# Performance work log

Hardware: AMD Instinct MI355X
Metric: run time of the kernel (lower is better)

Reference implementation:

```python
import jax, jax.numpy as jnp
import numpy as np

B, Q, L = 262144, 32, 8


def _rx(theta, ar, ai, br, bi):
    # RX(t) = [[cos(t/2), -i sin(t/2)], [-i sin(t/2), cos(t/2)]]
    c, s = jnp.cos(theta * 0.5), jnp.sin(theta * 0.5)
    return (c * ar + s * bi, c * ai - s * br,
            s * ai + c * br, -s * ar + c * bi)


def _ry(theta, ar, ai, br, bi):
    # RY(t) = [[cos(t/2), -sin(t/2)], [sin(t/2), cos(t/2)]] (real)
    c, s = jnp.cos(theta * 0.5), jnp.sin(theta * 0.5)
    return (c * ar - s * br, c * ai - s * bi,
            s * ar + c * br, s * ai + c * bi)


def _rz(theta, ar, ai, br, bi):
    # RZ(t) = diag(e^{-it/2}, e^{it/2})
    c, s = jnp.cos(theta * 0.5), jnp.sin(theta * 0.5)
    return (c * ar + s * ai, c * ai - s * ar,
            c * br - s * bi, c * bi + s * br)


def setup_inputs() -> dict:
    key = jax.random.key(0)
    k1, k2 = jax.random.split(key)
    x = jax.random.normal(k1, (B, Q), dtype=jnp.float32)
    params = jax.random.normal(k2, (L, Q, 3), dtype=jnp.float32)
    return {"x": x, "params": params}


def reference(x, params):
    # The circuit has only single-qubit gates, so the state factorizes into
    # an independent 2-amplitude state per (batch, qubit); track re/im parts.
    ar = jnp.ones_like(x)          # amplitude of |0>, real part
    ai = jnp.zeros_like(x)
    br = jnp.zeros_like(x)         # amplitude of |1>
    bi = jnp.zeros_like(x)
    # input encoding: RX(x_i) on wire i
    ar, ai, br, bi = _rx(x, ar, ai, br, bi)
    # trainable layers: RY, RZ, RX per qubit (broadcast over batch)
    for layer in range(params.shape[0]):
        ar, ai, br, bi = _ry(params[layer, :, 0][None, :], ar, ai, br, bi)
        ar, ai, br, bi = _rz(params[layer, :, 1][None, :], ar, ai, br, bi)
        ar, ai, br, bi = _rx(params[layer, :, 2][None, :], ar, ai, br, bi)
    # <Z> = |a|^2 - |b|^2 per (batch, qubit)
    return ar * ar + ai * ai - br * br - bi * bi
```

## Files before the change

### kernel.cpp

```cpp
#include <hip/hip_runtime.h>
#include <math.h>

#define NQ 32
#define MAXL 16

typedef float v4f __attribute__((ext_vector_type(4)));

struct Amp { float ar, ai, br, bi; };

__device__ __forceinline__ void g_ry(float c, float s, Amp& v) {
    Amp o;
    o.ar = c * v.ar - s * v.br;
    o.ai = c * v.ai - s * v.bi;
    o.br = s * v.ar + c * v.br;
    o.bi = s * v.ai + c * v.bi;
    v = o;
}
__device__ __forceinline__ void g_rz(float c, float s, Amp& v) {
    Amp o;
    o.ar = c * v.ar + s * v.ai;
    o.ai = c * v.ai - s * v.ar;
    o.br = c * v.br - s * v.bi;
    o.bi = c * v.bi + s * v.br;
    v = o;
}
__device__ __forceinline__ void g_rx(float c, float s, Amp& v) {
    Amp o;
    o.ar = c * v.ar + s * v.bi;
    o.ai = c * v.ai - s * v.br;
    o.br = s * v.ai + c * v.br;
    o.bi = -s * v.ar + c * v.bi;
    v = o;
}

__global__ __launch_bounds__(256, 8) void qc_fused(const float* __restrict__ x,
                                                   const float* __restrict__ params,
                                                   float* __restrict__ out,
                                                   int n4, int L) {
    __shared__ float sTh[MAXL * NQ * 3];
    __shared__ float sK[3][NQ];
    const int t = threadIdx.x;
    const int stride = gridDim.x * blockDim.x;
    const v4f* __restrict__ x4 = reinterpret_cast<const v4f*>(x);
    v4f* __restrict__ out4 = reinterpret_cast<v4f*>(out);

    const int i0 = blockIdx.x * blockDim.x + t;
    const int i1 = i0 + stride, i2 = i1 + stride, i3 = i2 + stride;
    const bool h0 = i0 < n4, h1 = i1 < n4, h2 = i2 < n4, h3 = i3 < n4;
    v4f xa = {0,0,0,0}, xb = {0,0,0,0}, xc = {0,0,0,0}, xd = {0,0,0,0};
    if (h0) xa = x4[i0];
    if (h1) xb = x4[i1];
    if (h2) xc = x4[i2];
    if (h3) xd = x4[i3];

    const int nTh4 = (L * NQ * 3) / 4;
    for (int j = t; j < nTh4; j += blockDim.x)
        reinterpret_cast<v4f*>(sTh)[j] = reinterpret_cast<const v4f*>(params)[j];
    __syncthreads();

    if (t < NQ) {
        Amp e0 = {1.f, 0.f, 0.f, 0.f};
        Amp e1 = {0.f, 0.f, 1.f, 0.f};
        for (int l = 0; l < L; ++l) {
            const float* th = &sTh[(l * NQ + t) * 3];
            float c, s;
            __sincosf(th[0] * 0.5f, &s, &c);
            g_ry(c, s, e0); g_ry(c, s, e1);
            __sincosf(th[1] * 0.5f, &s, &c);
            g_rz(c, s, e0); g_rz(c, s, e1);
            __sincosf(th[2] * 0.5f, &s, &c);
            g_rx(c, s, e0); g_rx(c, s, e1);
        }
        float A = (e0.ar * e0.ar + e0.ai * e0.ai) - (e0.br * e0.br + e0.bi * e0.bi);
        float B = (e1.ar * e1.ar + e1.ai * e1.ai) - (e1.br * e1.br + e1.bi * e1.bi);
        float C = 2.f * ((e0.ar * e1.ai - e0.ai * e1.ar) -
                         (e0.br * e1.bi - e0.bi * e1.br));
        sK[0][t] = 0.5f * (A + B);
        sK[1][t] = 0.5f * (A - B);
        sK[2][t] = 0.5f * C;
    }
    __syncthreads();

    const int q = (4 * t) & (NQ - 1);
    const float k0a = sK[0][q + 0], k1a = sK[1][q + 0], k2a = sK[2][q + 0];
    const float k0b = sK[0][q + 1], k1b = sK[1][q + 1], k2b = sK[2][q + 1];
    const float k0c = sK[0][q + 2], k1c = sK[1][q + 2], k2c = sK[2][q + 2];
    const float k0d = sK[0][q + 3], k1d = sK[1][q + 3], k2d = sK[2][q + 3];

#define EVAL(xv, ov)                                                        \
    do {                                                                    \
        float s_, c_;                                                       \
        __sincosf((xv)[0], &s_, &c_); (ov)[0] = fmaf(k1a, c_, fmaf(k2a, s_, k0a)); \
        __sincosf((xv)[1], &s_, &c_); (ov)[1] = fmaf(k1b, c_, fmaf(k2b, s_, k0b)); \
        __sincosf((xv)[2], &s_, &c_); (ov)[2] = fmaf(k1c, c_, fmaf(k2c, s_, k0c)); \
        __sincosf((xv)[3], &s_, &c_); (ov)[3] = fmaf(k1d, c_, fmaf(k2d, s_, k0d)); \
    } while (0)

    v4f o;
    if (h0) { EVAL(xa, o); __builtin_nontemporal_store(o, out4 + i0); }
    if (h1) { EVAL(xb, o); __builtin_nontemporal_store(o, out4 + i1); }
    if (h2) { EVAL(xc, o); __builtin_nontemporal_store(o, out4 + i2); }
    if (h3) { EVAL(xd, o); __builtin_nontemporal_store(o, out4 + i3); }

    for (int i = i3 + stride; i < n4; i += stride) {
        v4f xv = x4[i];
        EVAL(xv, o);
        __builtin_nontemporal_store(o, out4 + i);
    }
#undef EVAL
}

extern "C" void kernel_launch(void* const* d_in, const int* in_sizes, int n_in,
                              void* d_out, int out_size, void* d_ws, size_t ws_size,
                              hipStream_t stream) {
    const float* x      = (const float*)d_in[0];
    const float* params = (const float*)d_in[1];
    float* out          = (float*)d_out;

    int L  = in_sizes[1] / (NQ * 3);
    if (L > MAXL) L = MAXL;
    int n  = in_sizes[0];
    int n4 = n / 4;

    int block = 256;
    int grid  = 2048;
    qc_fused<<<grid, block, 0, stream>>>(x, params, out, n4, L);
}
```

Baseline: 15.17 us.

## Use amplitude-phase cosine form, nontemporal loads, and 1024-thread blocks

Rewrites the per-element output k0 + k1*cos + k2*sin as k0 + R*cos(x - phi), with R and phi computed once per qubit, so each element needs one cosine instead of a sincos. The two basis-state simulations are split across 64 lanes and combined with a cross-lane shuffle. Input loads become nontemporal, and the launch changes to 1024-thread blocks with a 512-block grid, still 4 float4 per thread. Risks are small accuracy changes from atan2 and the phase subtraction, and the params copy now assumes one block can load every parameter vector in a single pass.

```diff
diff --git a/kernel.cpp b/kernel.cpp
--- a/kernel.cpp
+++ b/kernel.cpp
@@ -33,12 +33,12 @@
     v = o;
 }
 
-__global__ __launch_bounds__(256, 8) void qc_fused(const float* __restrict__ x,
-                                                   const float* __restrict__ params,
-                                                   float* __restrict__ out,
-                                                   int n4, int L) {
+__global__ __launch_bounds__(1024, 8) void qc_fused(const float* __restrict__ x,
+                                                    const float* __restrict__ params,
+                                                    float* __restrict__ out,
+                                                    int n4, int L) {
     __shared__ float sTh[MAXL * NQ * 3];
-    __shared__ float sK[3][NQ];
+    __shared__ float sK0[NQ], sR[NQ], sPh[NQ];
     const int t = threadIdx.x;
     const int stride = gridDim.x * blockDim.x;
     const v4f* __restrict__ x4 = reinterpret_cast<const v4f*>(x);
@@ -48,52 +48,61 @@
     const int i1 = i0 + stride, i2 = i1 + stride, i3 = i2 + stride;
     const bool h0 = i0 < n4, h1 = i1 < n4, h2 = i2 < n4, h3 = i3 < n4;
     v4f xa = {0,0,0,0}, xb = {0,0,0,0}, xc = {0,0,0,0}, xd = {0,0,0,0};
-    if (h0) xa = x4[i0];
-    if (h1) xb = x4[i1];
-    if (h2) xc = x4[i2];
-    if (h3) xd = x4[i3];
+    if (h0) xa = __builtin_nontemporal_load(x4 + i0);
+    if (h1) xb = __builtin_nontemporal_load(x4 + i1);
+    if (h2) xc = __builtin_nontemporal_load(x4 + i2);
+    if (h3) xd = __builtin_nontemporal_load(x4 + i3);
 
     const int nTh4 = (L * NQ * 3) / 4;
-    for (int j = t; j < nTh4; j += blockDim.x)
-        reinterpret_cast<v4f*>(sTh)[j] = reinterpret_cast<const v4f*>(params)[j];
+    if (t < nTh4)
+        reinterpret_cast<v4f*>(sTh)[t] = reinterpret_cast<const v4f*>(params)[t];
     __syncthreads();
 
-    if (t < NQ) {
-        Amp e0 = {1.f, 0.f, 0.f, 0.f};
-        Amp e1 = {0.f, 0.f, 1.f, 0.f};
+    if (t < 64) {
+        const int q = t & (NQ - 1);
+        Amp v;
+        if (t < NQ) v = {1.f, 0.f, 0.f, 0.f};
+        else        v = {0.f, 0.f, 1.f, 0.f};
         for (int l = 0; l < L; ++l) {
-            const float* th = &sTh[(l * NQ + t) * 3];
+            const float* th = &sTh[(l * NQ + q) * 3];
             float c, s;
             __sincosf(th[0] * 0.5f, &s, &c);
-            g_ry(c, s, e0); g_ry(c, s, e1);
+            g_ry(c, s, v);
             __sincosf(th[1] * 0.5f, &s, &c);
-            g_rz(c, s, e0); g_rz(c, s, e1);
+            g_rz(c, s, v);
             __sincosf(th[2] * 0.5f, &s, &c);
-            g_rx(c, s, e0); g_rx(c, s, e1);
+            g_rx(c, s, v);
         }
-        float A = (e0.ar * e0.ar + e0.ai * e0.ai) - (e0.br * e0.br + e0.bi * e0.bi);
-        float B = (e1.ar * e1.ar + e1.ai * e1.ai) - (e1.br * e1.br + e1.bi * e1.bi);
-        float C = 2.f * ((e0.ar * e1.ai - e0.ai * e1.ar) -
-                         (e0.br * e1.bi - e0.bi * e1.br));
-        sK[0][t] = 0.5f * (A + B);
-        sK[1][t] = 0.5f * (A - B);
-        sK[2][t] = 0.5f * C;
+        float par = __shfl_xor(v.ar, 32);
+        float pai = __shfl_xor(v.ai, 32);
+        float pbr = __shfl_xor(v.br, 32);
+        float pbi = __shfl_xor(v.bi, 32);
+        if (t < NQ) {
+            float A = (v.ar * v.ar + v.ai * v.ai) - (v.br * v.br + v.bi * v.bi);
+            float B = (par * par + pai * pai) - (pbr * pbr + pbi * pbi);
+            float C = 2.f * ((v.ar * pai - v.ai * par) - (v.br * pbi - v.bi * pbr));
+            float K0 = 0.5f * (A + B);
+            float K1 = 0.5f * (A - B);
+            float K2 = 0.5f * C;
+            sK0[q] = K0;
+            sR[q]  = sqrtf(K1 * K1 + K2 * K2);
+            sPh[q] = atan2f(K2, K1);
+        }
     }
     __syncthreads();
 
     const int q = (4 * t) & (NQ - 1);
-    const float k0a = sK[0][q + 0], k1a = sK[1][q + 0], k2a = sK[2][q + 0];
-    const float k0b = sK[0][q + 1], k1b = sK[1][q + 1], k2b = sK[2][q + 1];
-    const float k0c = sK[0][q + 2], k1c = sK[1][q + 2], k2c = sK[2][q + 2];
-    const float k0d = sK[0][q + 3], k1d = sK[1][q + 3], k2d = sK[2][q + 3];
+    const float k0a = sK0[q + 0], ra = sR[q + 0], pa = sPh[q + 0];
+    const float k0b = sK0[q + 1], rb = sR[q + 1], pb = sPh[q + 1];
+    const float k0c = sK0[q + 2], rc = sR[q + 2], pc = sPh[q + 2];
+    const float k0d = sK0[q + 3], rd = sR[q + 3], pd = sPh[q + 3];
 
-#define EVAL(xv, ov)                                                        \
-    do {                                                                    \
-        float s_, c_;                                                       \
-        __sincosf((xv)[0], &s_, &c_); (ov)[0] = fmaf(k1a, c_, fmaf(k2a, s_, k0a)); \
-        __sincosf((xv)[1], &s_, &c_); (ov)[1] = fmaf(k1b, c_, fmaf(k2b, s_, k0b)); \
-        __sincosf((xv)[2], &s_, &c_); (ov)[2] = fmaf(k1c, c_, fmaf(k2c, s_, k0c)); \
-        __sincosf((xv)[3], &s_, &c_); (ov)[3] = fmaf(k1d, c_, fmaf(k2d, s_, k0d)); \
+#define EVAL(xv, ov)                                            \
+    do {                                                        \
+        (ov)[0] = fmaf(ra, __cosf((xv)[0] - pa), k0a);          \
+        (ov)[1] = fmaf(rb, __cosf((xv)[1] - pb), k0b);          \
+        (ov)[2] = fmaf(rc, __cosf((xv)[2] - pc), k0c);          \
+        (ov)[3] = fmaf(rd, __cosf((xv)[3] - pd), k0d);          \
     } while (0)
 
     v4f o;
@@ -103,7 +112,7 @@
     if (h3) { EVAL(xd, o); __builtin_nontemporal_store(o, out4 + i3); }
 
     for (int i = i3 + stride; i < n4; i += stride) {
-        v4f xv = x4[i];
+        v4f xv = __builtin_nontemporal_load(x4 + i);
         EVAL(xv, o);
         __builtin_nontemporal_store(o, out4 + i);
     }
@@ -122,7 +131,7 @@
     int n  = in_sizes[0];
     int n4 = n / 4;
 
-    int block = 256;
-    int grid  = 2048;
+    int block = 1024;
+    int grid  = 512;
     qc_fused<<<grid, block, 0, stream>>>(x, params, out, n4, L);
 }
```

Result: faster. 13.86 us (-8.6%).
